# Performance work log

Hardware: AMD Instinct MI355X
Metric: run time of the kernel (lower is better)

Reference implementation:

```python
import jax, jax.numpy as jnp
import numpy as np

N_C = 50000
N_N = 50000
E = 500000
D = 128


def _graph_conv(x_src, src, dst, n_src, n_dst, W, b):
    # DGL GraphConv, norm='both': symmetric degree normalization, then linear.
    ones = jnp.ones(src.shape, x_src.dtype)
    deg_out = jax.ops.segment_sum(ones, src, num_segments=n_src)
    deg_in = jax.ops.segment_sum(ones, dst, num_segments=n_dst)
    norm_src = jnp.maximum(deg_out, 1.0) ** -0.5  # [n_src]
    norm_dst = jnp.maximum(deg_in, 1.0) ** -0.5   # [n_dst]
    m = (x_src * norm_src[:, None])[src]          # [E, D] gather
    agg = jax.ops.segment_sum(m, dst, num_segments=n_dst)  # [n_dst, D]
    return (agg * norm_dst[:, None]) @ W + b


def _sage_conv(x_src, x_dst, src, dst, n_dst, W_self, W_neigh, b):
    # DGL SAGEConv, aggregator='mean': fc_self(h_dst) + fc_neigh(mean_neigh) + bias.
    ones = jnp.ones(src.shape, x_src.dtype)
    deg_in = jnp.maximum(jax.ops.segment_sum(ones, dst, num_segments=n_dst), 1.0)
    h_neigh = jax.ops.segment_sum(x_src[src], dst, num_segments=n_dst) / deg_in[:, None]
    return x_dst @ W_self + h_neigh @ W_neigh + b


def setup_inputs() -> dict:
    key = jax.random.key(0)
    ks = jax.random.split(key, 20)
    s = 1.0 / np.sqrt(D)
    inp = {
        'feat_C': jax.random.normal(ks[0], (N_C, D), jnp.float32),
        'feat_N': jax.random.normal(ks[1], (N_N, D), jnp.float32),
        'W1_cc': jax.random.normal(ks[2], (D, D), jnp.float32) * s,
        'b1_cc': jnp.zeros((D,), jnp.float32),
        'W1_cn': jax.random.normal(ks[3], (D, D), jnp.float32) * s,
        'b1_cn': jnp.zeros((D,), jnp.float32),
        'W1_self': jax.random.normal(ks[4], (D, D), jnp.float32) * s,
        'W1_neigh': jax.random.normal(ks[5], (D, D), jnp.float32) * s,
        'b1_nn': jnp.zeros((D,), jnp.float32),
        'W2_cc': jax.random.normal(ks[6], (D, D), jnp.float32) * s,
        'b2_cc': jnp.zeros((D,), jnp.float32),
        'W2_cn': jax.random.normal(ks[7], (D, D), jnp.float32) * s,
        'b2_cn': jnp.zeros((D,), jnp.float32),
        'W2_self': jax.random.normal(ks[8], (D, D), jnp.float32) * s,
        'W2_neigh': jax.random.normal(ks[9], (D, D), jnp.float32) * s,
        'b2_nn': jnp.zeros((D,), jnp.float32),
        'cc_src': jax.random.randint(ks[10], (E,), 0, N_C),
        'cc_dst': jax.random.randint(ks[11], (E,), 0, N_C),
        'cn_src': jax.random.randint(ks[12], (E,), 0, N_C),
        'cn_dst': jax.random.randint(ks[13], (E,), 0, N_N),
        'nn_src': jax.random.randint(ks[14], (E,), 0, N_N),
        'nn_dst': jax.random.randint(ks[15], (E,), 0, N_N),
    }
    return inp


def reference(feat_C, feat_N, W1_cc, b1_cc, W1_cn, b1_cn, W1_self, W1_neigh, b1_nn,
              W2_cc, b2_cc, W2_cn, b2_cn, W2_self, W2_neigh, b2_nn,
              cc_src, cc_dst, cn_src, cn_dst, nn_src, nn_dst):
    # layer 1 (HeteroGraphConv, aggregate='sum') + relu
    hC = _graph_conv(feat_C, cc_src, cc_dst, N_C, N_C, W1_cc, b1_cc)
    hN = (_graph_conv(feat_C, cn_src, cn_dst, N_C, N_N, W1_cn, b1_cn)
          + _sage_conv(feat_N, feat_N, nn_src, nn_dst, N_N, W1_self, W1_neigh, b1_nn))
    hC = jax.nn.relu(hC)
    hN = jax.nn.relu(hN)
    # layer 2
    oC = _graph_conv(hC, cc_src, cc_dst, N_C, N_C, W2_cc, b2_cc)
    oN = (_graph_conv(hC, cn_src, cn_dst, N_C, N_N, W2_cn, b2_cn)
          + _sage_conv(hN, hN, nn_src, nn_dst, N_N, W2_self, W2_neigh, b2_nn))
    return oC, oN
```

## Files before the change

### kernel.cpp

```cpp
#include <hip/hip_runtime.h>

#define NCN 50000
#define NE  500000
#define DF  128

#define BSHIFT 9
#define NBUCK 98
#define BK 128
#define CAP 7168
#define CHUNK 4096

typedef __attribute__((ext_vector_type(8))) short mfrag;
typedef __attribute__((ext_vector_type(4))) float facc4;

__device__ inline ushort f2bf(float x) {
    unsigned u = __float_as_uint(x);
    unsigned r = (u + 0x7FFFu + ((u >> 16) & 1u)) >> 16;
    return (ushort)r;
}
__device__ inline float bf2f(ushort h) { return __uint_as_float(((unsigned)h) << 16); }

__device__ inline void store_split4(ushort* __restrict__ T, int row, int lane4,
                                    float4 v) {
    ushort h0 = f2bf(v.x); ushort l0 = f2bf(v.x - bf2f(h0));
    ushort h1 = f2bf(v.y); ushort l1 = f2bf(v.y - bf2f(h1));
    ushort h2 = f2bf(v.z); ushort l2 = f2bf(v.z - bf2f(h2));
    ushort h3 = f2bf(v.w); ushort l3 = f2bf(v.w - bf2f(h3));
    uint2 hp = make_uint2((uint)h0 | ((uint)h1 << 16), (uint)h2 | ((uint)h3 << 16));
    uint2 lp = make_uint2((uint)l0 | ((uint)l1 << 16), (uint)l2 | ((uint)l3 << 16));
    *(uint2*)(T + (size_t)row * DF + lane4 * 4) = hp;
    *(uint2*)(T + (size_t)NCN * DF + (size_t)row * DF + lane4 * 4) = lp;
}

__global__ __launch_bounds__(256) void hist2_k(
    const int* __restrict__ cc_src, const int* __restrict__ cn_src,
    int* __restrict__ cnt2)
{
    int i = blockIdx.x * 256 + threadIdx.x;
    if (i >= NE) return;
    atomicAdd(&cnt2[cc_src[i]], 1);
    atomicAdd(&cnt2[NCN + cn_src[i]], 1);
}

__global__ __launch_bounds__(256) void srcnorm_k(
    const int* __restrict__ cnt2, float* __restrict__ snorm2, int n2)
{
    int i = blockIdx.x * 256 + threadIdx.x;
    if (i >= n2) return;
    int c = cnt2[i]; if (c < 1) c = 1;
    snorm2[i] = rsqrtf((float)c);
}

__global__ __launch_bounds__(256) void binA_k(
    const int* __restrict__ cc_src, const int* __restrict__ cc_dst,
    const int* __restrict__ cn_src, const int* __restrict__ cn_dst,
    const int* __restrict__ nn_src, const int* __restrict__ nn_dst,
    uint2* __restrict__ R, int* __restrict__ bc)
{
    const int s = blockIdx.y;
    const int* key; const int* pay;
    switch (s) {
      case 0: key = cc_dst; pay = cc_src; break;
      case 1: key = cn_dst; pay = cn_src; break;
      default: key = nn_dst; pay = nn_src; break;
    }
    __shared__ uint2 rec[CHUNK];
    __shared__ int lhist[BK], lofs[BK], lcur[BK], gbase[BK];
    __shared__ int ls[256];
    const int tid = threadIdx.x;
    const int base = blockIdx.x * CHUNK;

    int k[16], p[16];
    #pragma unroll
    for (int j = 0; j < 16; ++j) {
        int e = base + j * 256 + tid;
        bool valid = (e < NE);
        k[j] = valid ? key[e] : -1;
        p[j] = valid ? pay[e] : 0;
    }
    if (tid < BK) lhist[tid] = 0;
    __syncthreads();
    #pragma unroll
    for (int j = 0; j < 16; ++j)
        if (k[j] >= 0) atomicAdd(&lhist[k[j] >> BSHIFT], 1);
    __syncthreads();
    int v = (tid < BK) ? lhist[tid] : 0;
    ls[tid] = v;
    __syncthreads();
    #pragma unroll
    for (int off = 1; off < 128; off <<= 1) {
        int t = (tid >= off) ? ls[tid - off] : 0;
        __syncthreads();
        ls[tid] += t;
        __syncthreads();
    }
    if (tid < BK) { int e = ls[tid] - v; lofs[tid] = e; lcur[tid] = e; }
    __syncthreads();
    #pragma unroll
    for (int j = 0; j < 16; ++j) {
        if (k[j] >= 0) {
            int b = k[j] >> BSHIFT;
            int pos = atomicAdd(&lcur[b], 1);
            rec[pos] = make_uint2((unsigned)k[j], (unsigned)p[j]);
        }
    }
    __syncthreads();
    if (tid < BK) {
        int c = lcur[tid] - lofs[tid];
        gbase[tid] = (c > 0) ? atomicAdd(&bc[s * BK + tid], c) : 0;
    }
    __syncthreads();
    int total = ls[127];
    for (int i = tid; i < total; i += 256) {
        uint2 r = rec[i];
        int b = (int)(r.x >> BSHIFT);
        int gi = gbase[b] + (i - lofs[b]);
        R[((size_t)s * NBUCK + b) * CAP + gi] = r;
    }
}

__global__ __launch_bounds__(256) void binB_k(
    const uint2* __restrict__ R, const int* __restrict__ bc,
    int* __restrict__ rp3, int* __restrict__ col3)
{
    const int b = blockIdx.x;
    const int s = blockIdx.y;
    const int tid = threadIdx.x;
    __shared__ int cnt[512];
    __shared__ int lofs[512];
    __shared__ int ls[256];
    __shared__ int sbase;

    const int nrec = bc[s * BK + b];
    const uint2* rec = R + ((size_t)s * NBUCK + b) * CAP;

    for (int i = tid; i < 512; i += 256) cnt[i] = 0;
    __syncthreads();
    for (int i = tid; i < nrec; i += 256)
        atomicAdd(&cnt[rec[i].x & 511], 1);
    __syncthreads();

    {
        int v = (tid < b) ? bc[s * BK + tid] : 0;
        ls[tid] = v;
        __syncthreads();
        for (int off = 128; off > 0; off >>= 1) {
            if (tid < off) ls[tid] += ls[tid + off];
            __syncthreads();
        }
        if (tid == 0) sbase = ls[0];
        __syncthreads();
    }
    const int colBase = sbase;

    int v0 = cnt[2 * tid], v1 = cnt[2 * tid + 1];
    int pairSum = v0 + v1;
    ls[tid] = pairSum;
    __syncthreads();
    #pragma unroll
    for (int off = 1; off < 256; off <<= 1) {
        int t = (tid >= off) ? ls[tid - off] : 0;
        __syncthreads();
        ls[tid] += t;
        __syncthreads();
    }
    int excl = ls[tid] - pairSum;
    lofs[2 * tid] = excl;
    lofs[2 * tid + 1] = excl + v0;
    __syncthreads();
    const int total = ls[255];

    int* rp = rp3 + (size_t)s * (NCN + 1);
    for (int j = tid; j < 512; j += 256) {
        int d = b * 512 + j;
        if (d < NCN) rp[d] = colBase + lofs[j];
    }
    if (b == NBUCK - 1 && tid == 0) rp[NCN] = colBase + total;
    __syncthreads();

    int* col = col3 + (size_t)s * NE + colBase;
    for (int i = tid; i < nrec; i += 256) {
        uint2 r = rec[i];
        int pos = atomicAdd(&lofs[r.x & 511], 1);
        col[pos] = (int)r.y;
    }
}

__global__ __launch_bounds__(256) void wconv_k(
    const float* __restrict__ Wm0, const float* __restrict__ Wm1,
    const float* __restrict__ Wm2, const float* __restrict__ Wm3,
    const float* __restrict__ Wm4, const float* __restrict__ Wm5,
    const float* __restrict__ Wm6, const float* __restrict__ Wm7,
    ushort* __restrict__ out)
{
    const float* Ws[8] = {Wm0, Wm1, Wm2, Wm3, Wm4, Wm5, Wm6, Wm7};
    const float* W = Ws[blockIdx.x];
    ushort* o = out + (size_t)blockIdx.x * 32768;
    for (int i = threadIdx.x; i < 16384; i += 256) {
        int c = i >> 13;
        int r = i & 8191;
        int n = r >> 6;
        int jj = r & 63;
        int kk = c * 64 + (jj ^ ((n & 7) << 3));
        float wv = W[kk * 128 + n];
        ushort h = f2bf(wv);
        float lv = wv - bf2f(h);
        o[c * 16384 + r] = h;
        o[c * 16384 + 8192 + r] = f2bf(lv);
    }
}

__global__ __launch_bounds__(256) void agg_k(
    const float* __restrict__ X0, const int* __restrict__ rp0,
    const int* __restrict__ col0, const float* __restrict__ sc0,
    ushort* __restrict__ out0,
    const float* __restrict__ X1, const int* __restrict__ rp1,
    const int* __restrict__ col1, const float* __restrict__ sc1,
    ushort* __restrict__ out1,
    const float* __restrict__ X2, const int* __restrict__ rp2,
    const int* __restrict__ col2, const float* __restrict__ sc2,
    ushort* __restrict__ out2)
{
    const float* X; const int* rp; const int* col; const float* sc; ushort* out;
    if (blockIdx.y == 0)      { X = X0; rp = rp0; col = col0; sc = sc0; out = out0; }
    else if (blockIdx.y == 1) { X = X1; rp = rp1; col = col1; sc = sc1; out = out1; }
    else                      { X = X2; rp = rp2; col = col2; sc = sc2; out = out2; }

    int wid = (blockIdx.x * 256 + threadIdx.x) >> 6;
    int half = (threadIdx.x >> 5) & 1;
    int lane4 = threadIdx.x & 31;
    int row = wid * 2 + half;
    if (row >= NCN) return;
    int e0 = rp[row], e1 = rp[row + 1];
    const bool useSc = (sc != nullptr);
    float4 a = make_float4(0.f, 0.f, 0.f, 0.f);
    int e = e0;
    while (e < e1) {
        int cnt = e1 - e; if (cnt > 32) cnt = 32;
        int myc = (lane4 < cnt) ? col[e + lane4] : 0;
        float mysc = (useSc && lane4 < cnt) ? sc[myc] : 1.0f;
        int j = 0;
        for (; j + 4 <= cnt; j += 4) {
            int s0 = __shfl(myc, j, 32),     s1 = __shfl(myc, j + 1, 32);
            int s2 = __shfl(myc, j + 2, 32), s3 = __shfl(myc, j + 3, 32);
            float c0 = __shfl(mysc, j, 32),     c1 = __shfl(mysc, j + 1, 32);
            float c2 = __shfl(mysc, j + 2, 32), c3 = __shfl(mysc, j + 3, 32);
            const float4 u0 = *(const float4*)(X + (size_t)s0 * DF + lane4 * 4);
            const float4 u1 = *(const float4*)(X + (size_t)s1 * DF + lane4 * 4);
            const float4 u2 = *(const float4*)(X + (size_t)s2 * DF + lane4 * 4);
            const float4 u3 = *(const float4*)(X + (size_t)s3 * DF + lane4 * 4);
            a.x = fmaf(u0.x, c0, a.x); a.y = fmaf(u0.y, c0, a.y);
            a.z = fmaf(u0.z, c0, a.z); a.w = fmaf(u0.w, c0, a.w);
            a.x = fmaf(u1.x, c1, a.x); a.y = fmaf(u1.y, c1, a.y);
            a.z = fmaf(u1.z, c1, a.z); a.w = fmaf(u1.w, c1, a.w);
            a.x = fmaf(u2.x, c2, a.x); a.y = fmaf(u2.y, c2, a.y);
            a.z = fmaf(u2.z, c2, a.z); a.w = fmaf(u2.w, c2, a.w);
            a.x = fmaf(u3.x, c3, a.x); a.y = fmaf(u3.y, c3, a.y);
            a.z = fmaf(u3.z, c3, a.z); a.w = fmaf(u3.w, c3, a.w);
        }
        for (; j < cnt; ++j) {
            int s0 = __shfl(myc, j, 32);
            float c0 = __shfl(mysc, j, 32);
            const float4 u0 = *(const float4*)(X + (size_t)s0 * DF + lane4 * 4);
            a.x = fmaf(u0.x, c0, a.x); a.y = fmaf(u0.y, c0, a.y);
            a.z = fmaf(u0.z, c0, a.z); a.w = fmaf(u0.w, c0, a.w);
        }
        e += cnt;
    }
    int deg = e1 - e0; if (deg < 1) deg = 1;
    float dsc = useSc ? rsqrtf((float)deg) : (1.0f / (float)deg);
    a.x *= dsc; a.y *= dsc; a.z *= dsc; a.w *= dsc;
    store_split4(out, row, lane4, a);
}

template<int NSRC, bool RELU, int F32S>
__global__ __launch_bounds__(256, 3) void mgemm_k(
    const void* __restrict__ A0, const void* __restrict__ A1, const void* __restrict__ A2,
    const ushort* __restrict__ Wi0, const ushort* __restrict__ Wi1, const ushort* __restrict__ Wi2,
    const float* __restrict__ b0, const float* __restrict__ b1,
    float* __restrict__ Y, int M)
{
    constexpr int NCH = 2 * NSRC;
    __shared__ ushort Wsm[16384];
    const int tid = threadIdx.x;
    const int l = tid & 63;
    const int wv = tid >> 6;
    const int r0 = blockIdx.x * 128;

    const void*   Aarr[3] = {A0, A1, A2};
    const ushort* Warr[3] = {Wi0, Wi1, Wi2};

    int arow[2];
    #pragma unroll
    for (int rt = 0; rt < 2; ++rt) {
        int r = r0 + wv * 32 + rt * 16 + (l & 15);
        arow[rt] = (r < M) ? r : (M - 1);
    }
    const int kgrp = (l >> 4) * 8;

    facc4 acc[2][8];
    #pragma unroll
    for (int rt = 0; rt < 2; ++rt)
        #pragma unroll
        for (int ct = 0; ct < 8; ++ct)
            acc[rt][ct] = (facc4){0.f, 0.f, 0.f, 0.f};

    uint4 Wr[8];
    auto loadWr = [&](int c) {
        int s = c >> 1, chalf = c & 1;
        const uint4* wp = (const uint4*)(Warr[s] + chalf * 16384);
        #pragma unroll
        for (int i = 0; i < 8; ++i) Wr[i] = wp[i * 256 + tid];
    };

    mfrag ahA[2][2], alA[2][2], ahB[2][2], alB[2][2];
    auto loadA = [&](int c, mfrag (&ah)[2][2], mfrag (&al)[2][2]) {
        int s = c >> 1;
        int k0 = (c & 1) * 64;
        if (s == F32S) {
            const float* F = (const float*)Aarr[s];
            #pragma unroll
            for (int ks = 0; ks < 2; ++ks)
                #pragma unroll
                for (int rt = 0; rt < 2; ++rt) {
                    const float* p = F + (size_t)arow[rt] * DF + k0 + ks * 32 + kgrp;
                    float4 v0 = *(const float4*)p;
                    float4 v1 = *(const float4*)(p + 4);
                    union { mfrag m; ushort u[8]; } H, L;
                    float vv0[4] = {v0.x, v0.y, v0.z, v0.w};
                    float vv1[4] = {v1.x, v1.y, v1.z, v1.w};
                    #pragma unroll
                    for (int j = 0; j < 4; ++j) {
                        ushort h = f2bf(vv0[j]);
                        H.u[j] = h; L.u[j] = f2bf(vv0[j] - bf2f(h));
                    }
                    #pragma unroll
                    for (int j = 0; j < 4; ++j) {
                        ushort h = f2bf(vv1[j]);
                        H.u[4 + j] = h; L.u[4 + j] = f2bf(vv1[j] - bf2f(h));
                    }
                    ah[ks][rt] = H.m; al[ks][rt] = L.m;
                }
        } else {
            const ushort* T = (const ushort*)Aarr[s];
            #pragma unroll
            for (int ks = 0; ks < 2; ++ks)
                #pragma unroll
                for (int rt = 0; rt < 2; ++rt) {
                    size_t o = (size_t)arow[rt] * DF + k0 + ks * 32 + kgrp;
                    ah[ks][rt] = *(const mfrag*)(T + o);
                    al[ks][rt] = *(const mfrag*)(T + (size_t)NCN * DF + o);
                }
        }
    };

    auto compute = [&](const mfrag (&ah)[2][2], const mfrag (&al)[2][2]) {
        #pragma unroll
        for (int ks = 0; ks < 2; ++ks) {
            const int kbyte = ks * 64 + (l >> 4) * 16;
            #pragma unroll
            for (int ct = 0; ct < 8; ++ct) {
                int colc = ct * 16 + (l & 15);
                int widx = colc * 64 + ((kbyte ^ ((colc & 7) << 4)) >> 1);
                mfrag w_hi = *(const mfrag*)(Wsm + widx);
                mfrag w_lo = *(const mfrag*)(Wsm + 8192 + widx);
                #pragma unroll
                for (int rt = 0; rt < 2; ++rt) {
                    acc[rt][ct] = __builtin_amdgcn_mfma_f32_16x16x32_bf16(ah[ks][rt], w_hi, acc[rt][ct], 0, 0, 0);
                    acc[rt][ct] = __builtin_amdgcn_mfma_f32_16x16x32_bf16(ah[ks][rt], w_lo, acc[rt][ct], 0, 0, 0);
                    acc[rt][ct] = __builtin_amdgcn_mfma_f32_16x16x32_bf16(al[ks][rt], w_hi, acc[rt][ct], 0, 0, 0);
                }
            }
        }
    };

    loadWr(0);
    loadA(0, ahA, alA);
    #pragma unroll
    for (int c = 0; c < NCH; ++c) {
        __syncthreads();
        {
            uint4* wd = (uint4*)Wsm;
            #pragma unroll
            for (int i = 0; i < 8; ++i) wd[i * 256 + tid] = Wr[i];
        }
        if (c + 1 < NCH) {
            loadWr(c + 1);
            if ((c & 1) == 0) loadA(c + 1, ahB, alB);
            else              loadA(c + 1, ahA, alA);
        }
        __syncthreads();
        if ((c & 1) == 0) compute(ahA, alA);
        else              compute(ahB, alB);
    }
    __syncthreads();

    float bias[8];
    #pragma unroll
    for (int ct = 0; ct < 8; ++ct) {
        int colc = ct * 16 + (l & 15);
        float bv = b0 ? b0[colc] : 0.f;
        if (b1) bv += b1[colc];
        bias[ct] = bv;
    }
    #pragma unroll
    for (int rt = 0; rt < 2; ++rt) {
        #pragma unroll
        for (int q = 0; q < 4; ++q) {
            int row = r0 + wv * 32 + rt * 16 + (l >> 4) * 4 + q;
            if (row < M) {
                #pragma unroll
                for (int ct = 0; ct < 8; ++ct) {
                    float v = acc[rt][ct][q] + bias[ct];
                    if (RELU) v = fmaxf(v, 0.f);
                    Y[(size_t)row * DF + ct * 16 + (l & 15)] = v;
                }
            }
        }
    }
}

extern "C" void kernel_launch(void* const* d_in, const int* in_sizes, int n_in,
                              void* d_out, int out_size, void* d_ws, size_t ws_size,
                              hipStream_t stream)
{
    (void)in_sizes; (void)n_in; (void)out_size; (void)ws_size;
    const float* feat_C   = (const float*)d_in[0];
    const float* feat_N   = (const float*)d_in[1];
    const float* W1_cc    = (const float*)d_in[2];
    const float* b1_cc    = (const float*)d_in[3];
    const float* W1_cn    = (const float*)d_in[4];
    const float* b1_cn    = (const float*)d_in[5];
    const float* W1_self  = (const float*)d_in[6];
    const float* W1_neigh = (const float*)d_in[7];
    const float* b1_nn    = (const float*)d_in[8];
    const float* W2_cc    = (const float*)d_in[9];
    const float* b2_cc    = (const float*)d_in[10];
    const float* W2_cn    = (const float*)d_in[11];
    const float* b2_cn    = (const float*)d_in[12];
    const float* W2_self  = (const float*)d_in[13];
    const float* W2_neigh = (const float*)d_in[14];
    const float* b2_nn    = (const float*)d_in[15];
    const int* cc_src = (const int*)d_in[16];
    const int* cc_dst = (const int*)d_in[17];
    const int* cn_src = (const int*)d_in[18];
    const int* cn_dst = (const int*)d_in[19];
    const int* nn_src = (const int*)d_in[20];
    const int* nn_dst = (const int*)d_in[21];

    char* ws = (char*)d_ws;
    size_t off = 0;
    auto take = [&](size_t bytes) -> char* {
        char* p = ws + off;
        off = (off + bytes + 255) & ~(size_t)255;
        return p;
    };
    int*    rp3    = (int*)take((size_t)3 * (NCN + 1) * sizeof(int));
    int*    col3   = (int*)take((size_t)3 * NE * sizeof(int));
    float*  snorm2 = (float*)take((size_t)2 * NCN * sizeof(float));
    int*    cnt2   = (int*)take((size_t)2 * NCN * sizeof(int));
    int*    bc     = (int*)take((size_t)3 * BK * sizeof(int));
    ushort* Wimg   = (ushort*)take((size_t)8 * 32768 * sizeof(ushort));
    char* bigRegion = take((size_t)2 * 2 * NCN * DF * sizeof(ushort));
    uint2*  R  = (uint2*)bigRegion;
    ushort* P0 = (ushort*)bigRegion;
    ushort* P1 = (ushort*)(bigRegion + (size_t)2 * NCN * DF * sizeof(ushort));

    float* oC = (float*)d_out;
    float* oN = oC + (size_t)NCN * DF;
    ushort* oCsplit = (ushort*)oC;

    const int edgeBlocks = (NE + 255) / 256;
    const int binABlocks = (NE + CHUNK - 1) / CHUNK;
    const int aggBlocks  = (((NCN + 1) / 2) * 64 + 255) / 256;
    const int gemmBlocks = (NCN + 127) / 128;

    auto img = [&](int m) { return (const ushort*)(Wimg + (size_t)m * 32768); };
    const int* rpCC = rp3 + 0 * (NCN + 1);
    const int* rpCN = rp3 + 1 * (NCN + 1);
    const int* rpNN = rp3 + 2 * (NCN + 1);
    const int* colCC = col3 + 0 * NE;
    const int* colCN = col3 + 1 * NE;
    const int* colNN = col3 + 2 * NE;
    const float* snCC = snorm2 + 0 * NCN;
    const float* snCN = snorm2 + 1 * NCN;

    hipMemsetAsync(cnt2, 0, (size_t)2 * NCN * sizeof(int), stream);
    hipMemsetAsync(bc, 0, (size_t)3 * BK * sizeof(int), stream);
    hist2_k<<<edgeBlocks, 256, 0, stream>>>(cc_src, cn_src, cnt2);
    srcnorm_k<<<(2 * NCN + 255) / 256, 256, 0, stream>>>(cnt2, snorm2, 2 * NCN);
    binA_k<<<dim3(binABlocks, 3), 256, 0, stream>>>(cc_src, cc_dst, cn_src, cn_dst,
                                                    nn_src, nn_dst, R, bc);
    binB_k<<<dim3(NBUCK, 3), 256, 0, stream>>>(R, bc, rp3, col3);
    wconv_k<<<8, 256, 0, stream>>>(W1_cc, W1_cn, W1_neigh, W1_self,
                                   W2_cc, W2_cn, W2_neigh, W2_self, Wimg);

    agg_k<<<dim3(aggBlocks, 3), 256, 0, stream>>>(
        feat_C, rpCC, colCC, snCC, P0,
        feat_C, rpCN, colCN, snCN, P1,
        feat_N, rpNN, colNN, nullptr, oCsplit);
    mgemm_k<3, true, 2><<<gemmBlocks, 256, 0, stream>>>(P1, oCsplit, feat_N,
                                                        img(1), img(2), img(3),
                                                        b1_cn, b1_nn, oN, NCN);
    mgemm_k<1, true, -1><<<gemmBlocks, 256, 0, stream>>>(P0, nullptr, nullptr,
                                                         img(0), nullptr, nullptr,
                                                         b1_cc, nullptr, oC, NCN);

    agg_k<<<dim3(aggBlocks, 2), 256, 0, stream>>>(
        oC, rpCC, colCC, snCC, P0,
        oC, rpCN, colCN, snCN, P1,
        nullptr, nullptr, nullptr, nullptr, nullptr);
    agg_k<<<dim3(aggBlocks, 1), 256, 0, stream>>>(
        oN, rpNN, colNN, nullptr, oCsplit,
        nullptr, nullptr, nullptr, nullptr, nullptr,
        nullptr, nullptr, nullptr, nullptr, nullptr);
    mgemm_k<3, false, 2><<<gemmBlocks, 256, 0, stream>>>(P1, oCsplit, oN,
                                                         img(5), img(6), img(7),
                                                         b2_cn, b2_nn, oN, NCN);
    mgemm_k<1, false, -1><<<gemmBlocks, 256, 0, stream>>>(P0, nullptr, nullptr,
                                                          img(4), nullptr, nullptr,
                                                          b2_cc, nullptr, oC, NCN);
}
```

Measured before the change: 465.6 us.

## Interleave split-bf16 NN aggregate in place and fuse layer-1 GEMMs into one launch

The mean-neighbour aggregate is stored as interleaved hi/lo bf16 rows inside the destination fp32 buffer. Each GEMM row then reads and overwrites only its own footprint, which frees oC so the layer-1 N-type and C-type GEMMs can run in a single launch over a z dimension. The GEMM body also drops A-fragment double buffering, presumably to cut register pressure, and changes launch bounds from 3 to 2 blocks per SM. The trade-off is less load/compute overlap inside the GEMM in exchange for fewer launches and more concurrent blocks.

```diff
diff --git a/kernel.cpp b/kernel.cpp
--- a/kernel.cpp
+++ b/kernel.cpp
@@ -20,16 +20,19 @@
 }
 __device__ inline float bf2f(ushort h) { return __uint_as_float(((unsigned)h) << 16); }
 
-__device__ inline void store_split4(ushort* __restrict__ T, int row, int lane4,
-                                    float4 v) {
+__device__ inline void store_split4m(ushort* __restrict__ T, int row, int lane4,
+                                     float4 v, int mode) {
     ushort h0 = f2bf(v.x); ushort l0 = f2bf(v.x - bf2f(h0));
     ushort h1 = f2bf(v.y); ushort l1 = f2bf(v.y - bf2f(h1));
     ushort h2 = f2bf(v.z); ushort l2 = f2bf(v.z - bf2f(h2));
     ushort h3 = f2bf(v.w); ushort l3 = f2bf(v.w - bf2f(h3));
     uint2 hp = make_uint2((uint)h0 | ((uint)h1 << 16), (uint)h2 | ((uint)h3 << 16));
     uint2 lp = make_uint2((uint)l0 | ((uint)l1 << 16), (uint)l2 | ((uint)l3 << 16));
-    *(uint2*)(T + (size_t)row * DF + lane4 * 4) = hp;
-    *(uint2*)(T + (size_t)NCN * DF + (size_t)row * DF + lane4 * 4) = lp;
+    size_t hiOff, loOff;
+    if (mode == 0) { hiOff = (size_t)row * DF; loOff = (size_t)NCN * DF + (size_t)row * DF; }
+    else           { hiOff = (size_t)row * 256; loOff = hiOff + 128; }
+    *(uint2*)(T + hiOff + lane4 * 4) = hp;
+    *(uint2*)(T + loOff + lane4 * 4) = lp;
 }
 
 __global__ __launch_bounds__(256) void hist2_k(
@@ -213,18 +216,18 @@
 __global__ __launch_bounds__(256) void agg_k(
     const float* __restrict__ X0, const int* __restrict__ rp0,
     const int* __restrict__ col0, const float* __restrict__ sc0,
-    ushort* __restrict__ out0,
+    ushort* __restrict__ out0, int m0,
     const float* __restrict__ X1, const int* __restrict__ rp1,
     const int* __restrict__ col1, const float* __restrict__ sc1,
-    ushort* __restrict__ out1,
+    ushort* __restrict__ out1, int m1,
     const float* __restrict__ X2, const int* __restrict__ rp2,
     const int* __restrict__ col2, const float* __restrict__ sc2,
-    ushort* __restrict__ out2)
-{
-    const float* X; const int* rp; const int* col; const float* sc; ushort* out;
-    if (blockIdx.y == 0)      { X = X0; rp = rp0; col = col0; sc = sc0; out = out0; }
-    else if (blockIdx.y == 1) { X = X1; rp = rp1; col = col1; sc = sc1; out = out1; }
-    else                      { X = X2; rp = rp2; col = col2; sc = sc2; out = out2; }
+    ushort* __restrict__ out2, int m2)
+{
+    const float* X; const int* rp; const int* col; const float* sc; ushort* out; int mode;
+    if (blockIdx.y == 0)      { X = X0; rp = rp0; col = col0; sc = sc0; out = out0; mode = m0; }
+    else if (blockIdx.y == 1) { X = X1; rp = rp1; col = col1; sc = sc1; out = out1; mode = m1; }
+    else                      { X = X2; rp = rp2; col = col2; sc = sc2; out = out2; mode = m2; }
 
     int wid = (blockIdx.x * 256 + threadIdx.x) >> 6;
     int half = (threadIdx.x >> 5) & 1;
@@ -270,22 +273,23 @@
     int deg = e1 - e0; if (deg < 1) deg = 1;
     float dsc = useSc ? rsqrtf((float)deg) : (1.0f / (float)deg);
     a.x *= dsc; a.y *= dsc; a.z *= dsc; a.w *= dsc;
-    store_split4(out, row, lane4, a);
-}
-
-template<int NSRC, bool RELU, int F32S>
-__global__ __launch_bounds__(256, 3) void mgemm_k(
+    store_split4m(out, row, lane4, a, mode);
+}
+
+template<int NSRC, bool RELU, int F32S, bool A1INT>
+__device__ __forceinline__ void gemm_body(
+    ushort* __restrict__ Wsm,
     const void* __restrict__ A0, const void* __restrict__ A1, const void* __restrict__ A2,
     const ushort* __restrict__ Wi0, const ushort* __restrict__ Wi1, const ushort* __restrict__ Wi2,
     const float* __restrict__ b0, const float* __restrict__ b1,
-    float* __restrict__ Y, int M)
+    float* __restrict__ Y)
 {
     constexpr int NCH = 2 * NSRC;
-    __shared__ ushort Wsm[16384];
     const int tid = threadIdx.x;
     const int l = tid & 63;
     const int wv = tid >> 6;
     const int r0 = blockIdx.x * 128;
+    const int M = NCN;
 
     const void*   Aarr[3] = {A0, A1, A2};
     const ushort* Warr[3] = {Wi0, Wi1, Wi2};
@@ -313,8 +317,8 @@
         for (int i = 0; i < 8; ++i) Wr[i] = wp[i * 256 + tid];
     };
 
-    mfrag ahA[2][2], alA[2][2], ahB[2][2], alB[2][2];
-    auto loadA = [&](int c, mfrag (&ah)[2][2], mfrag (&al)[2][2]) {
+    mfrag ah[2][2], al[2][2];
+    auto loadA = [&](int c) {
         int s = c >> 1;
         int k0 = (c & 1) * 64;
         if (s == F32S) {
@@ -343,18 +347,32 @@
                 }
         } else {
             const ushort* T = (const ushort*)Aarr[s];
+            const bool INT = (s == 1 && A1INT);
+            const int rs = INT ? 256 : DF;
+            const size_t lo = INT ? 128 : (size_t)NCN * DF;
             #pragma unroll
             for (int ks = 0; ks < 2; ++ks)
                 #pragma unroll
                 for (int rt = 0; rt < 2; ++rt) {
-                    size_t o = (size_t)arow[rt] * DF + k0 + ks * 32 + kgrp;
+                    size_t o = (size_t)arow[rt] * rs + k0 + ks * 32 + kgrp;
                     ah[ks][rt] = *(const mfrag*)(T + o);
-                    al[ks][rt] = *(const mfrag*)(T + (size_t)NCN * DF + o);
+                    al[ks][rt] = *(const mfrag*)(T + o + lo);
                 }
         }
     };
 
-    auto compute = [&](const mfrag (&ah)[2][2], const mfrag (&al)[2][2]) {
+    loadWr(0);
+    #pragma unroll
+    for (int c = 0; c < NCH; ++c) {
+        __syncthreads();
+        {
+            uint4* wd = (uint4*)Wsm;
+            #pragma unroll
+            for (int i = 0; i < 8; ++i) wd[i * 256 + tid] = Wr[i];
+        }
+        loadA(c);
+        if (c + 1 < NCH) loadWr(c + 1);
+        __syncthreads();
         #pragma unroll
         for (int ks = 0; ks < 2; ++ks) {
             const int kbyte = ks * 64 + (l >> 4) * 16;
@@ -372,26 +390,6 @@
                 }
             }
         }
-    };
-
-    loadWr(0);
-    loadA(0, ahA, alA);
-    #pragma unroll
-    for (int c = 0; c < NCH; ++c) {
-        __syncthreads();
-        {
-            uint4* wd = (uint4*)Wsm;
-            #pragma unroll
-            for (int i = 0; i < 8; ++i) wd[i * 256 + tid] = Wr[i];
-        }
-        if (c + 1 < NCH) {
-            loadWr(c + 1);
-            if ((c & 1) == 0) loadA(c + 1, ahB, alB);
-            else              loadA(c + 1, ahA, alA);
-        }
-        __syncthreads();
-        if ((c & 1) == 0) compute(ahA, alA);
-        else              compute(ahB, alB);
     }
     __syncthreads();
 
@@ -418,6 +416,49 @@
             }
         }
     }
+}
+
+template<bool RELU>
+__global__ __launch_bounds__(256, 2) void fgemm2_k(
+    const ushort* __restrict__ AN0, const ushort* __restrict__ AN1i,
+    const float* __restrict__ AN2f,
+    const ushort* __restrict__ WiN0, const ushort* __restrict__ WiN1,
+    const ushort* __restrict__ WiN2,
+    const float* __restrict__ bN0, const float* __restrict__ bN1,
+    float* __restrict__ YN,
+    const ushort* __restrict__ AC0, const ushort* __restrict__ WiC,
+    const float* __restrict__ bC, float* __restrict__ YC)
+{
+    __shared__ ushort Wsm[16384];
+    if (blockIdx.z == 0)
+        gemm_body<3, RELU, 2, true>(Wsm, AN0, AN1i, AN2f, WiN0, WiN1, WiN2,
+                                    bN0, bN1, YN);
+    else
+        gemm_body<1, RELU, -1, false>(Wsm, AC0, nullptr, nullptr,
+                                      WiC, nullptr, nullptr, bC, nullptr, YC);
+}
+
+template<bool RELU>
+__global__ __launch_bounds__(256, 2) void gemmN_k(
+    const ushort* __restrict__ A0, const ushort* __restrict__ A1i,
+    const float* __restrict__ A2f,
+    const ushort* __restrict__ Wi0, const ushort* __restrict__ Wi1,
+    const ushort* __restrict__ Wi2,
+    const float* __restrict__ b0, const float* __restrict__ b1,
+    float* __restrict__ Y)
+{
+    __shared__ ushort Wsm[16384];
+    gemm_body<3, RELU, 2, true>(Wsm, A0, A1i, A2f, Wi0, Wi1, Wi2, b0, b1, Y);
+}
+
+template<bool RELU>
+__global__ __launch_bounds__(256, 2) void gemmC_k(
+    const ushort* __restrict__ A0, const ushort* __restrict__ Wi0,
+    const float* __restrict__ b0, float* __restrict__ Y)
+{
+    __shared__ ushort Wsm[16384];
+    gemm_body<1, RELU, -1, false>(Wsm, A0, nullptr, nullptr, Wi0, nullptr, nullptr,
+                                  b0, nullptr, Y);
 }
 
 extern "C" void kernel_launch(void* const* d_in, const int* in_sizes, int n_in,
@@ -468,7 +509,8 @@
 
     float* oC = (float*)d_out;
     float* oN = oC + (size_t)NCN * DF;
-    ushort* oCsplit = (ushort*)oC;
+    ushort* oC_us = (ushort*)oC;
+    ushort* oN_us = (ushort*)oN;
 
     const int edgeBlocks = (NE + 255) / 256;
     const int binABlocks = (NE + CHUNK - 1) / CHUNK;
@@ -496,28 +538,23 @@
                                    W2_cc, W2_cn, W2_neigh, W2_self, Wimg);
 
     agg_k<<<dim3(aggBlocks, 3), 256, 0, stream>>>(
-        feat_C, rpCC, colCC, snCC, P0,
-        feat_C, rpCN, colCN, snCN, P1,
-        feat_N, rpNN, colNN, nullptr, oCsplit);
-    mgemm_k<3, true, 2><<<gemmBlocks, 256, 0, stream>>>(P1, oCsplit, feat_N,
-                                                        img(1), img(2), img(3),
-                                                        b1_cn, b1_nn, oN, NCN);
-    mgemm_k<1, true, -1><<<gemmBlocks, 256, 0, stream>>>(P0, nullptr, nullptr,
-                                                         img(0), nullptr, nullptr,
-                                                         b1_cc, nullptr, oC, NCN);
+        feat_C, rpCC, colCC, snCC, P0, 0,
+        feat_C, rpCN, colCN, snCN, P1, 0,
+        feat_N, rpNN, colNN, nullptr, oN_us, 1);
+    fgemm2_k<true><<<dim3(gemmBlocks, 1, 2), 256, 0, stream>>>(
+        P1, oN_us, feat_N, img(1), img(2), img(3), b1_cn, b1_nn, oN,
+        P0, img(0), b1_cc, oC);
 
     agg_k<<<dim3(aggBlocks, 2), 256, 0, stream>>>(
-        oC, rpCC, colCC, snCC, P0,
-        oC, rpCN, colCN, snCN, P1,
-        nullptr, nullptr, nullptr, nullptr, nullptr);
+        oC, rpCC, colCC, snCC, P0, 0,
+        oC, rpCN, colCN, snCN, P1, 0,
+        nullptr, nullptr, nullptr, nullptr, nullptr, 0);
     agg_k<<<dim3(aggBlocks, 1), 256, 0, stream>>>(
-        oN, rpNN, colNN, nullptr, oCsplit,
-        nullptr, nullptr, nullptr, nullptr, nullptr,
-        nullptr, nullptr, nullptr, nullptr, nullptr);
-    mgemm_k<3, false, 2><<<gemmBlocks, 256, 0, stream>>>(P1, oCsplit, oN,
-                                                         img(5), img(6), img(7),
-                                                         b2_cn, b2_nn, oN, NCN);
-    mgemm_k<1, false, -1><<<gemmBlocks, 256, 0, stream>>>(P0, nullptr, nullptr,
-                                                          img(4), nullptr, nullptr,
-                                                          b2_cc, nullptr, oC, NCN);
-}
+        oN, rpNN, colNN, nullptr, oC_us, 1,
+        nullptr, nullptr, nullptr, nullptr, nullptr, 0,
+        nullptr, nullptr, nullptr, nullptr, nullptr, 0);
+    gemmN_k<false><<<gemmBlocks, 256, 0, stream>>>(P1, oC_us, oN,
+                                                   img(5), img(6), img(7),
+                                                   b2_cn, b2_nn, oN);
+    gemmC_k<false><<<gemmBlocks, 256, 0, stream>>>(P0, img(4), b2_cc, oC);
+}
```

After: 425.7 us. 8.6% less time.
